# Kernel tuning notes

Hardware: AMD Instinct MI355X
Metric: run time of the kernel (lower is better)

## Reference

```python
import jax, jax.numpy as jnp
import numpy as np

BN_EPS = 1e-5

def _ste_sign(x):
    # forward: sign in {-1,+1}; backward: clipped straight-through (grad 1 on [-1,1])
    s = jnp.where(x >= 0, 1.0, -1.0).astype(x.dtype)
    c = jnp.clip(x, -1.0, 1.0)
    return c + jax.lax.stop_gradient(s - c)

def setup_inputs() -> dict:
    key = jax.random.key(0)
    ks = jax.random.split(key, 8)
    N, C, H, W = 32, 256, 56, 56
    x = jax.random.normal(ks[0], (N, C, H, W), dtype=jnp.float32)
    bias0 = jax.random.normal(ks[1], (C,), dtype=jnp.float32) * 0.1
    w = jax.random.normal(ks[2], (C, C, 1, 1), dtype=jnp.float32) * 0.05
    gamma = jnp.ones((C,), dtype=jnp.float32)
    beta = jnp.zeros((C,), dtype=jnp.float32)
    bias1 = jax.random.normal(ks[3], (C,), dtype=jnp.float32) * 0.1
    alpha = jnp.full((C,), 0.25, dtype=jnp.float32)  # PReLU init
    bias2 = jax.random.normal(ks[4], (C,), dtype=jnp.float32) * 0.1
    return {"x": x, "bias0": bias0, "w": w, "gamma": gamma, "beta": beta,
            "bias1": bias1, "alpha": alpha, "bias2": bias2}

def reference(x, bias0, w, gamma, beta, bias1, alpha, bias2):
    ch = lambda v: v[None, :, None, None]
    # move0: learnable per-channel bias
    out = x + ch(bias0)
    # binary activation: sign (STE)
    out = _ste_sign(out)
    # binarized 1x1 conv: w_bin = mean(|w|) per out-channel * sign(w)
    scale = jnp.mean(jnp.abs(w), axis=(1, 2, 3))              # [O]
    wb = scale[:, None] * _ste_sign(w[:, :, 0, 0])            # [O, C]
    out = jnp.einsum('nchw,oc->nohw', out, wb)                # 1x1 conv
    # bn1: batch statistics (training-mode math)
    mu = jnp.mean(out, axis=(0, 2, 3), keepdims=True)
    var = jnp.var(out, axis=(0, 2, 3), keepdims=True)
    out = ch(gamma) * (out - mu) * jax.lax.rsqrt(var + BN_EPS) + ch(beta)
    # residual add (downsample is None)
    out = out + x
    # move1 -> PReLU -> move2
    out = out + ch(bias1)
    out = jnp.where(out > 0, out, ch(alpha) * out)
    out = out + ch(bias2)
    return out
```

## Files before the change

### kernel.cpp

```cpp
#include <hip/hip_runtime.h>
#include <stdint.h>

typedef unsigned long long u64;
typedef unsigned int u32;

constexpr int kC  = 256;
constexpr int kHW = 3136;
constexpr int kN  = 32;
constexpr int kP  = kN * kHW;
constexpr int kPosB = 128;
constexpr int kBlocksP = kP / kPosB;

constexpr size_t OFF_T     = 0;
constexpr size_t OFF_SCALE = 8192;
constexpr size_t OFF_SUMD  = 9216;
constexpr size_t OFF_SUMD2 = 11264;
constexpr size_t OFF_S     = 13312;

struct alignas(16) U64x2 { u64 x, y; };

__global__ __launch_bounds__(256) void prep_kernel(
    const float* __restrict__ w, char* __restrict__ ws) {
  u64*   T     = (u64*)(ws + OFF_T);
  float* scale = (float*)(ws + OFF_SCALE);
  u64*   sumd  = (u64*)(ws + OFF_SUMD);
  u64*   sumd2 = (u64*)(ws + OFF_SUMD2);

  int t = threadIdx.x;
  int k = t >> 6, lane = t & 63;
  int b = blockIdx.x;
  if (b == 0) { sumd[t] = 0ull; sumd2[t] = 0ull; }

  __shared__ float part[4][16];
#pragma unroll
  for (int i = 0; i < 16; ++i) {
    int o = b * 16 + i;
    float v = w[o * kC + k * 64 + lane];
    u64 m = __ballot(v >= 0.0f);
    float a = fabsf(v);
#pragma unroll
    for (int s = 32; s > 0; s >>= 1) a += __shfl_xor(a, s, 64);
    if (lane == 0) { T[k * 256 + o] = m; part[k][i] = a; }
  }
  __syncthreads();
  if (t < 16) {
    int o = b * 16 + t;
    scale[o] = (part[0][t] + part[1][t] + part[2][t] + part[3][t]) * (1.0f / 256.0f);
  }
}

__global__ __launch_bounds__(256) void pack_kernel(
    const float* __restrict__ x, const float* __restrict__ bias0,
    char* __restrict__ ws) {
  int t = threadIdx.x;
  int k = __builtin_amdgcn_readfirstlane(t >> 6);
  int lane = t & 63;

  u32 p  = blockIdx.x * (u32)kPosB + 2u * lane;
  u32 n  = p / kHW;
  u32 hw = p - n * kHW;
  const float* xp = x + (size_t)n * kC * kHW + (size_t)(k * 64) * kHW + hw;
  const float* bp = bias0 + k * 64;

  u64 m0 = 0, m1 = 0;
#pragma unroll 16
  for (int i = 0; i < 64; ++i) {
    float2 v = *(const float2*)(xp + (size_t)i * kHW);
    float bb = bp[i];
    m0 |= (u64)(v.x + bb >= 0.0f) << i;
    m1 |= (u64)(v.y + bb >= 0.0f) << i;
  }
  u64* S = (u64*)(ws + OFF_S);
  U64x2 st; st.x = m0; st.y = m1;
  *(U64x2*)&S[(size_t)k * kP + p] = st;
}

__global__ __launch_bounds__(256) void stats_kernel(char* __restrict__ ws) {
  int o = threadIdx.x;
  const u64* T = (const u64*)(ws + OFF_T);
  u64 t0 = T[o], t1 = T[256 + o], t2 = T[512 + o], t3 = T[768 + o];
  const u64* S = (const u64*)(ws + OFF_S);
  u32 pb = blockIdx.x * (u32)kPosB;

  int summ = 0, summ2 = 0;
#pragma unroll 8
  for (int j = 0; j < kPosB; j += 2) {
    u32 p = pb + j;
    U64x2 a0 = *(const U64x2*)&S[p];
    U64x2 a1 = *(const U64x2*)&S[kP + p];
    U64x2 a2 = *(const U64x2*)&S[2 * kP + p];
    U64x2 a3 = *(const U64x2*)&S[3 * kP + p];
    int ka = __popcll(a0.x ^ t0) + __popcll(a1.x ^ t1) +
             __popcll(a2.x ^ t2) + __popcll(a3.x ^ t3);
    int kb = __popcll(a0.y ^ t0) + __popcll(a1.y ^ t1) +
             __popcll(a2.y ^ t2) + __popcll(a3.y ^ t3);
    int ma = 128 - ka, mb = 128 - kb;
    summ  += ma + mb;
    summ2 += ma * ma + mb * mb;
  }
  atomicAdd((u64*)(ws + OFF_SUMD) + o,  (u64)(long long)(2 * summ));
  atomicAdd((u64*)(ws + OFF_SUMD2) + o, (u64)(long long)(4 * summ2));
}

__global__ __launch_bounds__(256) void finalize_kernel(
    const float* __restrict__ x, const float* __restrict__ gamma,
    const float* __restrict__ beta, const float* __restrict__ bias1,
    const float* __restrict__ alpha, const float* __restrict__ bias2,
    const char* __restrict__ ws, float* __restrict__ out) {
  __shared__ u64    ldsT[256][4];
  __shared__ float4 ldsC[256];

  int t = threadIdx.x;
  {
    const u64* T = (const u64*)(ws + OFF_T);
#pragma unroll
    for (int q = 0; q < 4; ++q) ldsT[t][q] = T[q * 256 + t];

    const float*     scale = (const float*)(ws + OFF_SCALE);
    const long long* sumd  = (const long long*)(ws + OFF_SUMD);
    const long long* sumd2 = (const long long*)(ws + OFF_SUMD2);
    double inv  = 1.0 / (double)kP;
    double md   = (double)sumd[t] * inv;
    double e2   = (double)sumd2[t] * inv;
    double vard = e2 - md * md;
    float sc  = scale[t];
    float mu  = sc * (float)md;
    float var = sc * sc * (float)vard;
    float rs  = rsqrtf(var + 1e-5f);
    float g   = gamma[t];
    float cA  = g * rs * sc;
    float cB  = beta[t] - g * rs * mu + bias1[t];
    ldsC[t] = make_float4(2.0f * cA, cB, alpha[t], bias2[t]);
  }
  __syncthreads();

  int k = __builtin_amdgcn_readfirstlane(t >> 6);
  int lane = t & 63;
  u32 p  = blockIdx.x * (u32)kPosB + 2u * lane;
  u32 n  = p / kHW;
  u32 hw = p - n * kHW;

  const u64* S = (const u64*)(ws + OFF_S);
  U64x2 s0 = *(const U64x2*)&S[p];
  U64x2 s1 = *(const U64x2*)&S[kP + p];
  U64x2 s2 = *(const U64x2*)&S[2 * kP + p];
  U64x2 s3 = *(const U64x2*)&S[3 * kP + p];

  const float* xp = x   + (size_t)n * kC * kHW + (size_t)(k * 64) * kHW + hw;
  float*       op = out + (size_t)n * kC * kHW + (size_t)(k * 64) * kHW + hw;

#pragma unroll 8
  for (int i = 0; i < 64; ++i) {
    int o = k * 64 + i;
    u64 w0 = ldsT[o][0], w1 = ldsT[o][1], w2 = ldsT[o][2], w3 = ldsT[o][3];
    int ka = __popcll(s0.x ^ w0) + __popcll(s1.x ^ w1) +
             __popcll(s2.x ^ w2) + __popcll(s3.x ^ w3);
    int kb = __popcll(s0.y ^ w0) + __popcll(s1.y ^ w1) +
             __popcll(s2.y ^ w2) + __popcll(s3.y ^ w3);
    float4 cc = ldsC[o];
    float2 xv = *(const float2*)(xp + (size_t)i * kHW);
    float u0 = fmaf(cc.x, (float)(128 - ka), cc.y) + xv.x;
    float u1 = fmaf(cc.x, (float)(128 - kb), cc.y) + xv.y;
    float r0 = u0 > 0.0f ? u0 : cc.z * u0;
    float r1 = u1 > 0.0f ? u1 : cc.z * u1;
    float2 ov; ov.x = r0 + cc.w; ov.y = r1 + cc.w;
    *(float2*)(op + (size_t)i * kHW) = ov;
  }
}

extern "C" void kernel_launch(void* const* d_in, const int* in_sizes, int n_in,
                              void* d_out, int out_size, void* d_ws, size_t ws_size,
                              hipStream_t stream) {
  const float* x     = (const float*)d_in[0];
  const float* bias0 = (const float*)d_in[1];
  const float* w     = (const float*)d_in[2];
  const float* gamma = (const float*)d_in[3];
  const float* beta  = (const float*)d_in[4];
  const float* bias1 = (const float*)d_in[5];
  const float* alpha = (const float*)d_in[6];
  const float* bias2 = (const float*)d_in[7];
  float* out = (float*)d_out;
  char*  ws  = (char*)d_ws;

  hipLaunchKernelGGL(prep_kernel, dim3(16), dim3(256), 0, stream, w, ws);
  hipLaunchKernelGGL(pack_kernel, dim3(kBlocksP), dim3(256), 0, stream,
                     x, bias0, ws);
  hipLaunchKernelGGL(stats_kernel, dim3(kBlocksP), dim3(256), 0, stream, ws);
  hipLaunchKernelGGL(finalize_kernel, dim3(kBlocksP), dim3(256), 0, stream,
                     x, gamma, beta, bias1, alpha, bias2, ws, out);
}
```

Before: 257.6 us.

## Fuse weight prep into pack kernel, halve positions per block, use nontemporal access

Folds the weight-binarization prep kernel into the first 16 blocks of the pack kernel, which removes one launch. Pack and finalize now handle one position per lane (64 positions per block, twice as many blocks) with scalar loads instead of float2. Streaming x reads and output writes use nontemporal loads and stores. Scalar accesses may coalesce less efficiently per instruction, though the doubled grid gives more parallelism. The fused prep has no ordering problem because stats and finalize run as later launches.

After: 242.3 us. 5.9% less time.

```diff
diff --git a/kernel.cpp b/kernel.cpp
--- a/kernel.cpp
+++ b/kernel.cpp
@@ -8,8 +8,10 @@
 constexpr int kHW = 3136;
 constexpr int kN  = 32;
 constexpr int kP  = kN * kHW;
-constexpr int kPosB = 128;
-constexpr int kBlocksP = kP / kPosB;
+constexpr int kPosPk = 64;
+constexpr int kBlkPk = kP / kPosPk;
+constexpr int kPosSt = 128;
+constexpr int kBlkSt = kP / kPosSt;
 
 constexpr size_t OFF_T     = 0;
 constexpr size_t OFF_SCALE = 8192;
@@ -19,60 +21,54 @@
 
 struct alignas(16) U64x2 { u64 x, y; };
 
-__global__ __launch_bounds__(256) void prep_kernel(
-    const float* __restrict__ w, char* __restrict__ ws) {
-  u64*   T     = (u64*)(ws + OFF_T);
-  float* scale = (float*)(ws + OFF_SCALE);
-  u64*   sumd  = (u64*)(ws + OFF_SUMD);
-  u64*   sumd2 = (u64*)(ws + OFF_SUMD2);
-
-  int t = threadIdx.x;
-  int k = t >> 6, lane = t & 63;
-  int b = blockIdx.x;
-  if (b == 0) { sumd[t] = 0ull; sumd2[t] = 0ull; }
-
-  __shared__ float part[4][16];
-#pragma unroll
-  for (int i = 0; i < 16; ++i) {
-    int o = b * 16 + i;
-    float v = w[o * kC + k * 64 + lane];
-    u64 m = __ballot(v >= 0.0f);
-    float a = fabsf(v);
-#pragma unroll
-    for (int s = 32; s > 0; s >>= 1) a += __shfl_xor(a, s, 64);
-    if (lane == 0) { T[k * 256 + o] = m; part[k][i] = a; }
-  }
-  __syncthreads();
-  if (t < 16) {
-    int o = b * 16 + t;
-    scale[o] = (part[0][t] + part[1][t] + part[2][t] + part[3][t]) * (1.0f / 256.0f);
-  }
-}
-
 __global__ __launch_bounds__(256) void pack_kernel(
     const float* __restrict__ x, const float* __restrict__ bias0,
-    char* __restrict__ ws) {
+    const float* __restrict__ w, char* __restrict__ ws) {
   int t = threadIdx.x;
-  int k = __builtin_amdgcn_readfirstlane(t >> 6);
+  int b = blockIdx.x;
+
+  if (b < 16) {
+    u64*   T     = (u64*)(ws + OFF_T);
+    float* scale = (float*)(ws + OFF_SCALE);
+    int kk = t >> 6, ln = t & 63;
+    if (b == 0) {
+      ((u64*)(ws + OFF_SUMD))[t]  = 0ull;
+      ((u64*)(ws + OFF_SUMD2))[t] = 0ull;
+    }
+    __shared__ float part[4][16];
+#pragma unroll
+    for (int i = 0; i < 16; ++i) {
+      int o = b * 16 + i;
+      float v = w[o * kC + kk * 64 + ln];
+      u64 m = __ballot(v >= 0.0f);
+      float a = fabsf(v);
+#pragma unroll
+      for (int s = 32; s > 0; s >>= 1) a += __shfl_xor(a, s, 64);
+      if (ln == 0) { T[kk * 256 + o] = m; part[kk][i] = a; }
+    }
+    __syncthreads();
+    if (t < 16) {
+      int o = b * 16 + t;
+      scale[o] = (part[0][t] + part[1][t] + part[2][t] + part[3][t]) * (1.0f / 256.0f);
+    }
+  }
+
+  int k    = __builtin_amdgcn_readfirstlane(t >> 6);
   int lane = t & 63;
-
-  u32 p  = blockIdx.x * (u32)kPosB + 2u * lane;
+  u32 p  = (u32)b * (u32)kPosPk + (u32)lane;
   u32 n  = p / kHW;
   u32 hw = p - n * kHW;
   const float* xp = x + (size_t)n * kC * kHW + (size_t)(k * 64) * kHW + hw;
   const float* bp = bias0 + k * 64;
 
-  u64 m0 = 0, m1 = 0;
-#pragma unroll 16
+  u64 m = 0;
+#pragma unroll 32
   for (int i = 0; i < 64; ++i) {
-    float2 v = *(const float2*)(xp + (size_t)i * kHW);
-    float bb = bp[i];
-    m0 |= (u64)(v.x + bb >= 0.0f) << i;
-    m1 |= (u64)(v.y + bb >= 0.0f) << i;
+    float v = __builtin_nontemporal_load(xp + (size_t)i * kHW) + bp[i];
+    m |= (u64)(v >= 0.0f) << i;
   }
   u64* S = (u64*)(ws + OFF_S);
-  U64x2 st; st.x = m0; st.y = m1;
-  *(U64x2*)&S[(size_t)k * kP + p] = st;
+  S[(size_t)k * kP + p] = m;
 }
 
 __global__ __launch_bounds__(256) void stats_kernel(char* __restrict__ ws) {
@@ -80,11 +76,11 @@
   const u64* T = (const u64*)(ws + OFF_T);
   u64 t0 = T[o], t1 = T[256 + o], t2 = T[512 + o], t3 = T[768 + o];
   const u64* S = (const u64*)(ws + OFF_S);
-  u32 pb = blockIdx.x * (u32)kPosB;
+  u32 pb = blockIdx.x * (u32)kPosSt;
 
   int summ = 0, summ2 = 0;
 #pragma unroll 8
-  for (int j = 0; j < kPosB; j += 2) {
+  for (int j = 0; j < kPosSt; j += 2) {
     u32 p = pb + j;
     U64x2 a0 = *(const U64x2*)&S[p];
     U64x2 a1 = *(const U64x2*)&S[kP + p];
@@ -134,17 +130,17 @@
   }
   __syncthreads();
 
-  int k = __builtin_amdgcn_readfirstlane(t >> 6);
+  int k    = __builtin_amdgcn_readfirstlane(t >> 6);
   int lane = t & 63;
-  u32 p  = blockIdx.x * (u32)kPosB + 2u * lane;
+  u32 p  = blockIdx.x * (u32)kPosPk + (u32)lane;
   u32 n  = p / kHW;
   u32 hw = p - n * kHW;
 
   const u64* S = (const u64*)(ws + OFF_S);
-  U64x2 s0 = *(const U64x2*)&S[p];
-  U64x2 s1 = *(const U64x2*)&S[kP + p];
-  U64x2 s2 = *(const U64x2*)&S[2 * kP + p];
-  U64x2 s3 = *(const U64x2*)&S[3 * kP + p];
+  u64 s0 = S[p];
+  u64 s1 = S[kP + p];
+  u64 s2 = S[2 * kP + p];
+  u64 s3 = S[3 * kP + p];
 
   const float* xp = x   + (size_t)n * kC * kHW + (size_t)(k * 64) * kHW + hw;
   float*       op = out + (size_t)n * kC * kHW + (size_t)(k * 64) * kHW + hw;
@@ -153,18 +149,13 @@
   for (int i = 0; i < 64; ++i) {
     int o = k * 64 + i;
     u64 w0 = ldsT[o][0], w1 = ldsT[o][1], w2 = ldsT[o][2], w3 = ldsT[o][3];
-    int ka = __popcll(s0.x ^ w0) + __popcll(s1.x ^ w1) +
-             __popcll(s2.x ^ w2) + __popcll(s3.x ^ w3);
-    int kb = __popcll(s0.y ^ w0) + __popcll(s1.y ^ w1) +
-             __popcll(s2.y ^ w2) + __popcll(s3.y ^ w3);
+    int kx = __popcll(s0 ^ w0) + __popcll(s1 ^ w1) +
+             __popcll(s2 ^ w2) + __popcll(s3 ^ w3);
     float4 cc = ldsC[o];
-    float2 xv = *(const float2*)(xp + (size_t)i * kHW);
-    float u0 = fmaf(cc.x, (float)(128 - ka), cc.y) + xv.x;
-    float u1 = fmaf(cc.x, (float)(128 - kb), cc.y) + xv.y;
-    float r0 = u0 > 0.0f ? u0 : cc.z * u0;
-    float r1 = u1 > 0.0f ? u1 : cc.z * u1;
-    float2 ov; ov.x = r0 + cc.w; ov.y = r1 + cc.w;
-    *(float2*)(op + (size_t)i * kHW) = ov;
+    float xv = __builtin_nontemporal_load(xp + (size_t)i * kHW);
+    float u  = fmaf(cc.x, (float)(128 - kx), cc.y) + xv;
+    float r  = u > 0.0f ? u : cc.z * u;
+    __builtin_nontemporal_store(r + cc.w, op + (size_t)i * kHW);
   }
 }
 
@@ -182,10 +173,9 @@
   float* out = (float*)d_out;
   char*  ws  = (char*)d_ws;
 
-  hipLaunchKernelGGL(prep_kernel, dim3(16), dim3(256), 0, stream, w, ws);
-  hipLaunchKernelGGL(pack_kernel, dim3(kBlocksP), dim3(256), 0, stream,
-                     x, bias0, ws);
-  hipLaunchKernelGGL(stats_kernel, dim3(kBlocksP), dim3(256), 0, stream, ws);
-  hipLaunchKernelGGL(finalize_kernel, dim3(kBlocksP), dim3(256), 0, stream,
+  hipLaunchKernelGGL(pack_kernel, dim3(kBlkPk), dim3(256), 0, stream,
+                     x, bias0, w, ws);
+  hipLaunchKernelGGL(stats_kernel, dim3(kBlkSt), dim3(256), 0, stream, ws);
+  hipLaunchKernelGGL(finalize_kernel, dim3(kBlkPk), dim3(256), 0, stream,
                      x, gamma, beta, bias1, alpha, bias2, ws, out);
 }
```
